# Optimization experiments

Measured on AMD Instinct MI355X. Metric: run time of the kernel, lower is better.

## Reference

```python
import jax, jax.numpy as jnp
import numpy as np

B, DIM_IN, T = 16, 512, 2048
DIM_OUT2 = 512 * 2  # dim_out * 2 (GLU halves it)
K = 3
STYLE = 128
SCALE_CONV = 1.0 / np.sqrt(DIM_IN * K ** 2).astype(np.float32)  # fan_in = dim_in * k^2 (as in source)
SCALE_LIN = 1.0 / np.sqrt(STYLE).astype(np.float32)


def setup_inputs() -> dict:
    key = jax.random.key(0)
    ks = jax.random.split(key, 6)
    x = jax.random.normal(ks[0], (B, DIM_IN, T), dtype=jnp.float32)
    c_src = jax.random.normal(ks[1], (B, STYLE), dtype=jnp.float32)
    c_trg = jax.random.normal(ks[2], (B, STYLE), dtype=jnp.float32)
    # EqualLinear params (lr_mul=1): weight ~ N(0,1), bias filled with bias_init=1
    w_s = jax.random.normal(ks[3], (DIM_IN, STYLE), dtype=jnp.float32)
    b_s = jnp.ones((DIM_IN,), dtype=jnp.float32)
    w_b = jax.random.normal(ks[4], (DIM_IN, STYLE), dtype=jnp.float32)
    b_b = jnp.ones((DIM_IN,), dtype=jnp.float32)
    weight = jax.random.normal(ks[5], (1, DIM_OUT2, DIM_IN, K), dtype=jnp.float32)
    return {"x": x, "c_src": c_src, "c_trg": c_trg,
            "w_s": w_s, "b_s": b_s, "w_b": w_b, "b_b": b_b, "weight": weight}


def reference(x, c_src, c_trg, w_s, b_s, w_b, b_b, weight):
    bsz, cin, t = x.shape
    cout = weight.shape[1]  # dim_out * 2
    k = weight.shape[3]
    # EqualLinear: F.linear(c, w*scale, bias)
    s = (c_trg @ (w_s * SCALE_LIN).T + b_s).reshape(bsz, 1, cin, 1)
    beta = (c_trg @ (w_b * SCALE_LIN).T + b_b).reshape(bsz, 1, cin, 1)
    w = SCALE_CONV * (weight * s + beta)               # [B, Cout, Cin, K]
    demod = jax.lax.rsqrt(jnp.sum(w * w, axis=(2, 3)) + 1e-8)   # [B, Cout]
    demod_mean = jnp.mean(w.reshape(bsz, cout, -1), axis=2)      # [B, Cout]
    w = (w - demod_mean[:, :, None, None]) * demod[:, :, None, None]
    # batch-as-groups conv1d
    w = w.reshape(bsz * cout, cin, k)
    xr = x.reshape(1, bsz * cin, t)
    out = jax.lax.conv_general_dilated(
        xr, w, window_strides=(1,), padding=[(k // 2, k // 2)],
        dimension_numbers=("NCH", "OIH", "NCH"), feature_group_count=bsz)
    out = out.reshape(bsz, cout, -1)
    a, g = jnp.split(out, 2, axis=1)  # GLU on channel dim
    return a * jax.nn.sigmoid(g)
```

## Files before the change

### kernel.cpp

```cpp
#include <hip/hip_runtime.h>
#include <math.h>

typedef __attribute__((ext_vector_type(8))) short short8;
typedef __attribute__((ext_vector_type(4))) float f32x4;
typedef unsigned short ushortT;

#define NB     16
#define CIN    512
#define TT     2048
#define COUT2  1024
#define NSTYLE 128
#define KKTOT  1536
#define TPAD   2050
#define NT32   48

#define SCALE_LIN  0.088388347648318447f
#define SCALE_CONV 0.014731391274719736f

__device__ __forceinline__ ushortT f2bf(float f) {
  union { float f; unsigned u; } v; v.f = f;
  unsigned r = v.u + 0x7fffu + ((v.u >> 16) & 1u);
  return (ushortT)(r >> 16);
}

__device__ __forceinline__ void gload16(const void* g, void* l) {
  __builtin_amdgcn_global_load_lds(
      (const __attribute__((address_space(1))) void*)g,
      (__attribute__((address_space(3))) void*)l, 16, 0, 0);
}

__global__ void style_kernel(const float* __restrict__ c_trg,
                             const float* __restrict__ w_s, const float* __restrict__ b_s,
                             const float* __restrict__ w_b, const float* __restrict__ b_b,
                             float* __restrict__ s, float* __restrict__ beta,
                             ushortT* __restrict__ xT) {
  int gid = blockIdx.x * 256 + threadIdx.x;
  int b = gid >> 9, ci = gid & 511;
  const float* ct = c_trg + b * NSTYLE;
  const float* ws = w_s + ci * NSTYLE;
  const float* wb = w_b + ci * NSTYLE;
  float as = 0.f, ab = 0.f;
#pragma unroll 8
  for (int j = 0; j < NSTYLE; ++j) {
    float c = ct[j];
    as += c * ws[j];
    ab += c * wb[j];
  }
  s[gid]    = as * SCALE_LIN + b_s[ci];
  beta[gid] = ab * SCALE_LIN + b_b[ci];
  xT[(size_t)b * TPAD * CIN + ci] = 0;
  xT[((size_t)b * TPAD + TPAD - 1) * CIN + ci] = 0;
}

__global__ void xpose_kernel(const float* __restrict__ x, ushortT* __restrict__ xT) {
  int b = blockIdx.z, ct = blockIdx.y, tt = blockIdx.x;
  int t0 = tt * 64, ci0 = ct * 64;
  __shared__ float tile[64][65];
  const float* xB = x + (size_t)b * CIN * TT;
  int rr = threadIdx.x >> 4;
  int c4 = threadIdx.x & 15;
#pragma unroll
  for (int it = 0; it < 4; ++it) {
    int ci = rr + it * 16;
    float4 v = *(const float4*)(xB + (size_t)(ci0 + ci) * TT + t0 + c4 * 4);
    tile[ci][c4 * 4 + 0] = v.x; tile[ci][c4 * 4 + 1] = v.y;
    tile[ci][c4 * 4 + 2] = v.z; tile[ci][c4 * 4 + 3] = v.w;
  }
  __syncthreads();
  ushortT* xTB = xT + (size_t)b * TPAD * CIN;
#pragma unroll
  for (int it = 0; it < 4; ++it) {
    int t = rr + it * 16;
    ushort4 o;
    o.x = f2bf(tile[c4 * 4 + 0][t]); o.y = f2bf(tile[c4 * 4 + 1][t]);
    o.z = f2bf(tile[c4 * 4 + 2][t]); o.w = f2bf(tile[c4 * 4 + 3][t]);
    *(ushort4*)(xTB + (size_t)(1 + t0 + t) * CIN + ci0 + c4 * 4) = o;
  }
}

__global__ void modw_kernel(const float* __restrict__ weight,
                            const float* __restrict__ s, const float* __restrict__ beta,
                            ushortT* __restrict__ wnorm) {
  int co = blockIdx.x, tid = threadIdx.x;
  int ci = tid * 2;
  const float* wp = weight + (size_t)co * KKTOT + (size_t)ci * 3;
  float2 va = *(const float2*)(wp);
  float2 vb = *(const float2*)(wp + 2);
  float2 vc = *(const float2*)(wp + 4);
  float v0 = va.x, v1 = va.y, v2 = vb.x, v3 = vb.y, v4 = vc.x, v5 = vc.y;
  int r = ((co & 511) << 1) | (co >> 9);
  __shared__ float rs[4], rq[4];
  for (int b = 0; b < NB; ++b) {
    float2 sv = *(const float2*)(s + b * CIN + ci);
    float2 ev = *(const float2*)(beta + b * CIN + ci);
    float w0 = SCALE_CONV * (v0 * sv.x + ev.x);
    float w1 = SCALE_CONV * (v1 * sv.x + ev.x);
    float w2 = SCALE_CONV * (v2 * sv.x + ev.x);
    float w3 = SCALE_CONV * (v3 * sv.y + ev.y);
    float w4 = SCALE_CONV * (v4 * sv.y + ev.y);
    float w5 = SCALE_CONV * (v5 * sv.y + ev.y);
    float sum = w0 + w1 + w2 + w3 + w4 + w5;
    float sq  = w0*w0 + w1*w1 + w2*w2 + w3*w3 + w4*w4 + w5*w5;
#pragma unroll
    for (int off = 32; off; off >>= 1) {
      sum += __shfl_xor(sum, off);
      sq  += __shfl_xor(sq,  off);
    }
    if ((tid & 63) == 0) { rs[tid >> 6] = sum; rq[tid >> 6] = sq; }
    __syncthreads();
    float mean  = (rs[0] + rs[1] + rs[2] + rs[3]) * (1.0f / 1536.0f);
    float demod = rsqrtf(rq[0] + rq[1] + rq[2] + rq[3] + 1e-8f);
    ushortT* dst = wnorm + ((size_t)b * COUT2 + r) * KKTOT;
    ushort2 p0, p1, p2;
    p0.x = f2bf((w0 - mean) * demod); p0.y = f2bf((w3 - mean) * demod);
    p1.x = f2bf((w1 - mean) * demod); p1.y = f2bf((w4 - mean) * demod);
    p2.x = f2bf((w2 - mean) * demod); p2.y = f2bf((w5 - mean) * demod);
    *(ushort2*)(dst +        ci) = p0;
    *(ushort2*)(dst +  512 + ci) = p1;
    *(ushort2*)(dst + 1024 + ci) = p2;
    __syncthreads();
  }
}


#define AFRAG(d, f) (*(const short8*)(ldsc + (d) * 24576 + aoff + (f) * 1024))
#define BFRAG(d, g) (*(const short8*)(ldsc + (d) * 24576 + 16384 + boff + (g) * 1024))

#define STAGE(dn, kt) do { int kc_ = (kt) * 32;                                 \
    gload16(sA0 + kc_, ldsw + (dn) * 12288 + dst8);                             \
    gload16(sA1 + kc_, ldsw + (dn) * 12288 + 4096 + dst8);                      \
    gload16(sB0 + kc_, ldsw + (dn) * 12288 + 8192 + dst8);                      \
  } while (0)

#define TILE(dc, ktn, DO_STAGE) do {                                            \
    short8 af0 = AFRAG(dc, 0), af1 = AFRAG(dc, 1);                              \
    short8 af2 = AFRAG(dc, 2), af3 = AFRAG(dc, 3);                              \
    short8 bf0 = BFRAG(dc, 0), bf1 = BFRAG(dc, 1);                              \
    short8 bf2 = BFRAG(dc, 2), bf3 = BFRAG(dc, 3);                              \
    if (DO_STAGE) STAGE((dc) ^ 1, ktn);                                         \
    __builtin_amdgcn_s_setprio(1);                                              \
    acc[0][0] = __builtin_amdgcn_mfma_f32_16x16x32_bf16(af0, bf0, acc[0][0], 0, 0, 0); \
    acc[0][1] = __builtin_amdgcn_mfma_f32_16x16x32_bf16(af0, bf1, acc[0][1], 0, 0, 0); \
    acc[0][2] = __builtin_amdgcn_mfma_f32_16x16x32_bf16(af0, bf2, acc[0][2], 0, 0, 0); \
    acc[0][3] = __builtin_amdgcn_mfma_f32_16x16x32_bf16(af0, bf3, acc[0][3], 0, 0, 0); \
    acc[1][0] = __builtin_amdgcn_mfma_f32_16x16x32_bf16(af1, bf0, acc[1][0], 0, 0, 0); \
    acc[1][1] = __builtin_amdgcn_mfma_f32_16x16x32_bf16(af1, bf1, acc[1][1], 0, 0, 0); \
    acc[1][2] = __builtin_amdgcn_mfma_f32_16x16x32_bf16(af1, bf2, acc[1][2], 0, 0, 0); \
    acc[1][3] = __builtin_amdgcn_mfma_f32_16x16x32_bf16(af1, bf3, acc[1][3], 0, 0, 0); \
    acc[2][0] = __builtin_amdgcn_mfma_f32_16x16x32_bf16(af2, bf0, acc[2][0], 0, 0, 0); \
    acc[2][1] = __builtin_amdgcn_mfma_f32_16x16x32_bf16(af2, bf1, acc[2][1], 0, 0, 0); \
    acc[2][2] = __builtin_amdgcn_mfma_f32_16x16x32_bf16(af2, bf2, acc[2][2], 0, 0, 0); \
    acc[2][3] = __builtin_amdgcn_mfma_f32_16x16x32_bf16(af2, bf3, acc[2][3], 0, 0, 0); \
    acc[3][0] = __builtin_amdgcn_mfma_f32_16x16x32_bf16(af3, bf0, acc[3][0], 0, 0, 0); \
    acc[3][1] = __builtin_amdgcn_mfma_f32_16x16x32_bf16(af3, bf1, acc[3][1], 0, 0, 0); \
    acc[3][2] = __builtin_amdgcn_mfma_f32_16x16x32_bf16(af3, bf2, acc[3][2], 0, 0, 0); \
    acc[3][3] = __builtin_amdgcn_mfma_f32_16x16x32_bf16(af3, bf3, acc[3][3], 0, 0, 0); \
    __builtin_amdgcn_s_setprio(0);                                              \
    __builtin_amdgcn_sched_barrier(0);                                          \
    asm volatile("s_waitcnt vmcnt(0)" ::: "memory");                            \
    __builtin_amdgcn_sched_barrier(0);                                          \
    __builtin_amdgcn_s_barrier();                                               \
    __builtin_amdgcn_sched_barrier(0);                                          \
  } while (0)

__global__ __launch_bounds__(512, 4)
void conv_gemm(const ushortT* __restrict__ wnorm, const ushortT* __restrict__ xT,
               float* __restrict__ out) {
  extern __shared__ ushortT ldsw[];
  const char* ldsc = (const char*)ldsw;

  int orig = blockIdx.x;
  int wgid = (orig & 7) * 128 + (orig >> 3);
  int b  = wgid >> 6;
  int mt = (wgid >> 4) & 3;
  int nt = wgid & 15;
  int co0 = mt * 256, t0 = nt * 128;

  int tid = threadIdx.x;
  int l = tid & 63, w = tid >> 6;
  int wm = w >> 1, wn = w & 1;

  int r0 = tid >> 2;
  int jbs8 = (((tid & 3) ^ ((r0 >> 1) & 3)) << 3);
  int dst8 = tid * 8;
  int cb = ((l >> 4) ^ ((l >> 1) & 3));
  int aoff = (wm * 64 + (l & 15)) * 64 + cb * 16;
  int boff = (wn * 64 + (l & 15)) * 64 + cb * 16;

  const ushortT* wB = wnorm + (size_t)b * COUT2 * KKTOT;
  const ushortT* xB = xT + (size_t)b * TPAD * CIN;
  const ushortT* sA0 = wB + (size_t)(co0 + r0) * KKTOT + jbs8;
  const ushortT* sA1 = sA0 + (size_t)128 * KKTOT;
  const ushortT* sB0 = xB + (size_t)(t0 + r0) * CIN + jbs8;

  f32x4 acc[4][4];
#pragma unroll
  for (int i = 0; i < 4; ++i)
#pragma unroll
    for (int j = 0; j < 4; ++j)
      acc[i][j] = (f32x4){0.f, 0.f, 0.f, 0.f};

  STAGE(0, 0);
  asm volatile("s_waitcnt vmcnt(0)" ::: "memory");
  __builtin_amdgcn_sched_barrier(0);
  __builtin_amdgcn_s_barrier();
  __builtin_amdgcn_sched_barrier(0);

  for (int j = 0; j < 23; ++j) {
    TILE(0, 2 * j + 1, 1);
    TILE(1, 2 * j + 2, 1);
  }
  TILE(0, 47, 1);
  TILE(1, 0, 0);

#pragma unroll
  for (int mi = 0; mi < 4; ++mi) {
    int cop = co0 + wm * 64 + mi * 16 + ((l >> 4) << 2);
    int c = cop >> 1;
    size_t obase = ((size_t)b * (COUT2 / 2) + c) * TT;
#pragma unroll
    for (int ni = 0; ni < 4; ++ni) {
      int t = t0 + wn * 64 + ni * 16 + (l & 15);
      f32x4 v = acc[mi][ni];
      out[obase + t]      = v.x / (1.f + __expf(-v.y));
      out[obase + TT + t] = v.z / (1.f + __expf(-v.w));
    }
  }
}

extern "C" void kernel_launch(void* const* d_in, const int* in_sizes, int n_in,
                              void* d_out, int out_size, void* d_ws, size_t ws_size,
                              hipStream_t stream) {
  const float* x      = (const float*)d_in[0];
  const float* c_trg  = (const float*)d_in[2];
  const float* w_s    = (const float*)d_in[3];
  const float* b_s    = (const float*)d_in[4];
  const float* w_b    = (const float*)d_in[5];
  const float* b_b    = (const float*)d_in[6];
  const float* weight = (const float*)d_in[7];
  float* out = (float*)d_out;

  char* ws = (char*)d_ws;
  float*   s     = (float*)ws;
  float*   beta  = (float*)(ws + 32768);
  ushortT* xT    = (ushortT*)(ws + 65536);
  ushortT* wnorm = (ushortT*)(ws + 65536 + 33587200);

  hipFuncSetAttribute((const void*)conv_gemm,
                      hipFuncAttributeMaxDynamicSharedMemorySize, 49152);

  style_kernel<<<32, 256, 0, stream>>>(c_trg, w_s, b_s, w_b, b_b, s, beta, xT);
  xpose_kernel<<<dim3(32, 8, 16), 256, 0, stream>>>(x, xT);
  modw_kernel<<<1024, 256, 0, stream>>>(weight, s, beta, wnorm);
  conv_gemm<<<1024, 512, 49152, stream>>>(wnorm, xT, out);
}
```

Before: 151.7 us.

## Enlarge GEMM tile to 256x256 with 4 waves and register double-buffered fragments

```diff
diff --git a/kernel.cpp b/kernel.cpp
--- a/kernel.cpp
+++ b/kernel.cpp
@@ -12,7 +12,6 @@
 #define NSTYLE 128
 #define KKTOT  1536
 #define TPAD   2050
-#define NT32   48
 
 #define SCALE_LIN  0.088388347648318447f
 #define SCALE_CONV 0.014731391274719736f
@@ -123,58 +122,53 @@
 }
 
 
-#define AFRAG(d, f) (*(const short8*)(ldsc + (d) * 24576 + aoff + (f) * 1024))
-#define BFRAG(d, g) (*(const short8*)(ldsc + (d) * 24576 + 16384 + boff + (g) * 1024))
-
-#define STAGE(dn, kt) do { int kc_ = (kt) * 32;                                 \
-    gload16(sA0 + kc_, ldsw + (dn) * 12288 + dst8);                             \
-    gload16(sA1 + kc_, ldsw + (dn) * 12288 + 4096 + dst8);                      \
-    gload16(sB0 + kc_, ldsw + (dn) * 12288 + 8192 + dst8);                      \
+#define AFRAG(d, f) (*(const short8*)(ldsc + (d) * 32768 + aoff + (f) * 1024))
+#define BFRAG(d, g) (*(const short8*)(ldsc + (d) * 32768 + 16384 + boff + (g) * 1024))
+
+#define STAGE(dn, kt) do { int kc_ = (kt) * 32;                                  \
+    gload16(sA0 + kc_,                ldsw + (dn) * 16384 + dst8);               \
+    gload16(sA0 + kc_ +  64 * KKTOT,  ldsw + (dn) * 16384 + 2048 + dst8);        \
+    gload16(sA0 + kc_ + 128 * KKTOT,  ldsw + (dn) * 16384 + 4096 + dst8);        \
+    gload16(sA0 + kc_ + 192 * KKTOT,  ldsw + (dn) * 16384 + 6144 + dst8);        \
+    gload16(sB0 + kc_,                ldsw + (dn) * 16384 + 8192 + dst8);        \
+    gload16(sB0 + kc_ +  64 * CIN,    ldsw + (dn) * 16384 + 10240 + dst8);       \
+    gload16(sB0 + kc_ + 128 * CIN,    ldsw + (dn) * 16384 + 12288 + dst8);       \
+    gload16(sB0 + kc_ + 192 * CIN,    ldsw + (dn) * 16384 + 14336 + dst8);       \
   } while (0)
 
-#define TILE(dc, ktn, DO_STAGE) do {                                            \
-    short8 af0 = AFRAG(dc, 0), af1 = AFRAG(dc, 1);                              \
-    short8 af2 = AFRAG(dc, 2), af3 = AFRAG(dc, 3);                              \
-    short8 bf0 = BFRAG(dc, 0), bf1 = BFRAG(dc, 1);                              \
-    short8 bf2 = BFRAG(dc, 2), bf3 = BFRAG(dc, 3);                              \
-    if (DO_STAGE) STAGE((dc) ^ 1, ktn);                                         \
-    __builtin_amdgcn_s_setprio(1);                                              \
-    acc[0][0] = __builtin_amdgcn_mfma_f32_16x16x32_bf16(af0, bf0, acc[0][0], 0, 0, 0); \
-    acc[0][1] = __builtin_amdgcn_mfma_f32_16x16x32_bf16(af0, bf1, acc[0][1], 0, 0, 0); \
-    acc[0][2] = __builtin_amdgcn_mfma_f32_16x16x32_bf16(af0, bf2, acc[0][2], 0, 0, 0); \
-    acc[0][3] = __builtin_amdgcn_mfma_f32_16x16x32_bf16(af0, bf3, acc[0][3], 0, 0, 0); \
-    acc[1][0] = __builtin_amdgcn_mfma_f32_16x16x32_bf16(af1, bf0, acc[1][0], 0, 0, 0); \
-    acc[1][1] = __builtin_amdgcn_mfma_f32_16x16x32_bf16(af1, bf1, acc[1][1], 0, 0, 0); \
-    acc[1][2] = __builtin_amdgcn_mfma_f32_16x16x32_bf16(af1, bf2, acc[1][2], 0, 0, 0); \
-    acc[1][3] = __builtin_amdgcn_mfma_f32_16x16x32_bf16(af1, bf3, acc[1][3], 0, 0, 0); \
-    acc[2][0] = __builtin_amdgcn_mfma_f32_16x16x32_bf16(af2, bf0, acc[2][0], 0, 0, 0); \
-    acc[2][1] = __builtin_amdgcn_mfma_f32_16x16x32_bf16(af2, bf1, acc[2][1], 0, 0, 0); \
-    acc[2][2] = __builtin_amdgcn_mfma_f32_16x16x32_bf16(af2, bf2, acc[2][2], 0, 0, 0); \
-    acc[2][3] = __builtin_amdgcn_mfma_f32_16x16x32_bf16(af2, bf3, acc[2][3], 0, 0, 0); \
-    acc[3][0] = __builtin_amdgcn_mfma_f32_16x16x32_bf16(af3, bf0, acc[3][0], 0, 0, 0); \
-    acc[3][1] = __builtin_amdgcn_mfma_f32_16x16x32_bf16(af3, bf1, acc[3][1], 0, 0, 0); \
-    acc[3][2] = __builtin_amdgcn_mfma_f32_16x16x32_bf16(af3, bf2, acc[3][2], 0, 0, 0); \
-    acc[3][3] = __builtin_amdgcn_mfma_f32_16x16x32_bf16(af3, bf3, acc[3][3], 0, 0, 0); \
-    __builtin_amdgcn_s_setprio(0);                                              \
-    __builtin_amdgcn_sched_barrier(0);                                          \
-    asm volatile("s_waitcnt vmcnt(0)" ::: "memory");                            \
-    __builtin_amdgcn_sched_barrier(0);                                          \
-    __builtin_amdgcn_s_barrier();                                               \
-    __builtin_amdgcn_sched_barrier(0);                                          \
+#define ITER(CA, CB, NA, NB_, RB, SB, KT, DOSTAGE, DOREAD) do {                  \
+    asm volatile("s_waitcnt vmcnt(0)" ::: "memory");                             \
+    __builtin_amdgcn_sched_barrier(0);                                           \
+    __builtin_amdgcn_s_barrier();                                                \
+    __builtin_amdgcn_sched_barrier(0);                                           \
+    if (DOREAD) {                                                                \
+      _Pragma("unroll") for (int f_ = 0; f_ < 8; ++f_) NA[f_]  = AFRAG(RB, f_);  \
+      _Pragma("unroll") for (int g_ = 0; g_ < 8; ++g_) NB_[g_] = BFRAG(RB, g_);  \
+    }                                                                            \
+    if (DOSTAGE) STAGE(SB, KT);                                                  \
+    __builtin_amdgcn_s_setprio(1);                                               \
+    _Pragma("unroll") for (int f_ = 0; f_ < 8; ++f_)                             \
+      _Pragma("unroll") for (int g_ = 0; g_ < 8; ++g_)                           \
+        acc[f_][g_] = __builtin_amdgcn_mfma_f32_16x16x32_bf16(                   \
+            CA[f_], CB[g_], acc[f_][g_], 0, 0, 0);                               \
+    __builtin_amdgcn_s_setprio(0);                                               \
+    __builtin_amdgcn_sched_barrier(0);                                           \
+    asm volatile("s_waitcnt lgkmcnt(0)" ::: "memory");                           \
+    __builtin_amdgcn_sched_barrier(0);                                           \
   } while (0)
 
-__global__ __launch_bounds__(512, 4)
+__global__ __launch_bounds__(256, 1)
 void conv_gemm(const ushortT* __restrict__ wnorm, const ushortT* __restrict__ xT,
                float* __restrict__ out) {
   extern __shared__ ushortT ldsw[];
   const char* ldsc = (const char*)ldsw;
 
   int orig = blockIdx.x;
-  int wgid = (orig & 7) * 128 + (orig >> 3);
-  int b  = wgid >> 6;
-  int mt = (wgid >> 4) & 3;
-  int nt = wgid & 15;
-  int co0 = mt * 256, t0 = nt * 128;
+  int wgid = (orig & 7) * 64 + (orig >> 3);
+  int b  = wgid >> 5;
+  int i5 = wgid & 31;
+  int mt = i5 >> 3, nt = i5 & 7;
+  int co0 = mt * 256, t0 = nt * 256;
 
   int tid = threadIdx.x;
   int l = tid & 63, w = tid >> 6;
@@ -184,44 +178,50 @@
   int jbs8 = (((tid & 3) ^ ((r0 >> 1) & 3)) << 3);
   int dst8 = tid * 8;
   int cb = ((l >> 4) ^ ((l >> 1) & 3));
-  int aoff = (wm * 64 + (l & 15)) * 64 + cb * 16;
-  int boff = (wn * 64 + (l & 15)) * 64 + cb * 16;
+  int aoff = (wm * 128 + (l & 15)) * 64 + cb * 16;
+  int boff = (wn * 128 + (l & 15)) * 64 + cb * 16;
 
   const ushortT* wB = wnorm + (size_t)b * COUT2 * KKTOT;
   const ushortT* xB = xT + (size_t)b * TPAD * CIN;
   const ushortT* sA0 = wB + (size_t)(co0 + r0) * KKTOT + jbs8;
-  const ushortT* sA1 = sA0 + (size_t)128 * KKTOT;
   const ushortT* sB0 = xB + (size_t)(t0 + r0) * CIN + jbs8;
 
-  f32x4 acc[4][4];
-#pragma unroll
-  for (int i = 0; i < 4; ++i)
-#pragma unroll
-    for (int j = 0; j < 4; ++j)
+  f32x4 acc[8][8];
+#pragma unroll
+  for (int i = 0; i < 8; ++i)
+#pragma unroll
+    for (int j = 0; j < 8; ++j)
       acc[i][j] = (f32x4){0.f, 0.f, 0.f, 0.f};
-
-  STAGE(0, 0);
-  asm volatile("s_waitcnt vmcnt(0)" ::: "memory");
+  short8 Xa[8], Xb[8], Ya[8], Yb[8];
+
+  STAGE(0, 0); STAGE(1, 1);
+  asm volatile("s_waitcnt vmcnt(8)" ::: "memory");
   __builtin_amdgcn_sched_barrier(0);
   __builtin_amdgcn_s_barrier();
   __builtin_amdgcn_sched_barrier(0);
-
-  for (int j = 0; j < 23; ++j) {
-    TILE(0, 2 * j + 1, 1);
-    TILE(1, 2 * j + 2, 1);
-  }
-  TILE(0, 47, 1);
-  TILE(1, 0, 0);
-
-#pragma unroll
-  for (int mi = 0; mi < 4; ++mi) {
-    int cop = co0 + wm * 64 + mi * 16 + ((l >> 4) << 2);
+#pragma unroll
+  for (int f = 0; f < 8; ++f) Xa[f] = AFRAG(0, f);
+#pragma unroll
+  for (int g = 0; g < 8; ++g) Xb[g] = BFRAG(0, g);
+  asm volatile("s_waitcnt lgkmcnt(0)" ::: "memory");
+  __builtin_amdgcn_sched_barrier(0);
+
+  for (int k2 = 0; k2 < 23; ++k2) {
+    ITER(Xa, Xb, Ya, Yb, 1, 0, 2 * k2 + 2, 1, 1);
+    ITER(Ya, Yb, Xa, Xb, 0, 1, 2 * k2 + 3, 1, 1);
+  }
+  ITER(Xa, Xb, Ya, Yb, 1, 0, 0, 0, 1);
+  ITER(Ya, Yb, Xa, Xb, 0, 0, 0, 0, 0);
+
+#pragma unroll
+  for (int f = 0; f < 8; ++f) {
+    int cop = co0 + wm * 128 + f * 16 + ((l >> 4) << 2);
     int c = cop >> 1;
     size_t obase = ((size_t)b * (COUT2 / 2) + c) * TT;
 #pragma unroll
-    for (int ni = 0; ni < 4; ++ni) {
-      int t = t0 + wn * 64 + ni * 16 + (l & 15);
-      f32x4 v = acc[mi][ni];
+    for (int g = 0; g < 8; ++g) {
+      int t = t0 + wn * 128 + g * 16 + (l & 15);
+      f32x4 v = acc[f][g];
       out[obase + t]      = v.x / (1.f + __expf(-v.y));
       out[obase + TT + t] = v.z / (1.f + __expf(-v.w));
     }
@@ -247,10 +247,10 @@
   ushortT* wnorm = (ushortT*)(ws + 65536 + 33587200);
 
   hipFuncSetAttribute((const void*)conv_gemm,
-                      hipFuncAttributeMaxDynamicSharedMemorySize, 49152);
+                      hipFuncAttributeMaxDynamicSharedMemorySize, 65536);
 
   style_kernel<<<32, 256, 0, stream>>>(c_trg, w_s, b_s, w_b, b_b, s, beta, xT);
   xpose_kernel<<<dim3(32, 8, 16), 256, 0, stream>>>(x, xT);
   modw_kernel<<<1024, 256, 0, stream>>>(weight, s, beta, wnorm);
-  conv_gemm<<<1024, 512, 49152, stream>>>(wnorm, xT, out);
-}
+  conv_gemm<<<512, 256, 65536, stream>>>(wnorm, xT, out);
+}
```

Measured after the change: 147.7 us. 2.6% less time.
